# Kernel optimization log

Measured on AMD Instinct MI355X. Metric: run time of the kernel, lower is better.

The kernel has to match this reference:

```python
import jax, jax.numpy as jnp
import numpy as np

N_NODES = 50000
N_EDGES = 1250000
D_FEAT = 64


def setup_inputs() -> dict:
    key = jax.random.key(0)
    k1, k2, k3, k4 = jax.random.split(key, 4)
    feat = jax.random.normal(k1, (N_NODES, D_FEAT), dtype=jnp.float32)
    edge_weight = jax.random.uniform(k2, (N_EDGES,), dtype=jnp.float32)
    edge_src = jax.random.randint(k3, (N_EDGES,), 0, N_NODES, dtype=jnp.int64)
    edge_dst = jnp.sort(jax.random.randint(k4, (N_EDGES,), 0, N_NODES, dtype=jnp.int64))
    return {"feat": feat, "edge_weight": edge_weight,
            "edge_src": edge_src, "edge_dst": edge_dst}


def reference(feat, edge_weight, edge_src, edge_dst):
    # u_mul_e: gather source node features, scale by per-edge weight
    msgs = feat[edge_src] * edge_weight[:, None]          # [E, d]
    # fn.sum: scatter-add messages to destination nodes
    rst = jax.ops.segment_sum(msgs, edge_dst, num_segments=N_NODES)  # [N, d]
    return rst
```

## Files before the change

kernel.cpp:

```cpp
#include <hip/hip_runtime.h>

#define D_FEAT 64

__global__ __launch_bounds__(256) void build_rowptr_scatter(
    const int* __restrict__ edge_dst, int* __restrict__ rp,
    int n_edges, int n_nodes) {
  const int e = blockIdx.x * blockDim.x + threadIdx.x;
  if (e > n_edges) return;
  const int d0 = (e == 0) ? -1 : edge_dst[e - 1];
  const int d1 = (e == n_edges) ? n_nodes : edge_dst[e];
  for (int v = d0 + 1; v <= d1; ++v) rp[v] = e;
}

__global__ __launch_bounds__(256) void gcn_gather4(
    const float* __restrict__ feat,
    const float* __restrict__ ew,
    const int* __restrict__ esrc,
    const int* __restrict__ rp,
    float* __restrict__ out, int n_nodes) {
  const int wave = (blockIdx.x * blockDim.x + threadIdx.x) >> 6;
  const int lane = threadIdx.x & 63;
  if (wave >= n_nodes) return;
  const int sub = lane >> 4;
  const int fl  = lane & 15;

  const int e0 = rp[wave];
  const int e1 = rp[wave + 1];

  float4 acc0 = {0.f, 0.f, 0.f, 0.f};
  float4 acc1 = {0.f, 0.f, 0.f, 0.f};

  const float4* feat4 = (const float4*)feat;

  for (int base = e0; base < e1; base += 64) {
    const int n = min(64, e1 - base);
    int   s = 0;
    float w = 0.0f;
    if (lane < n) {
      s = esrc[base + lane];
      w = ew[base + lane];
    }
    for (int i = 0; i < n; i += 8) {
      const int   sA = __shfl(s, i + sub);
      const float wA = __shfl(w, i + sub);
      const int   sB = __shfl(s, i + 4 + sub);
      const float wB = __shfl(w, i + 4 + sub);
      const float4 rA = feat4[(size_t)sA * 16 + fl];
      const float4 rB = feat4[(size_t)sB * 16 + fl];
      acc0.x = fmaf(rA.x, wA, acc0.x);
      acc0.y = fmaf(rA.y, wA, acc0.y);
      acc0.z = fmaf(rA.z, wA, acc0.z);
      acc0.w = fmaf(rA.w, wA, acc0.w);
      acc1.x = fmaf(rB.x, wB, acc1.x);
      acc1.y = fmaf(rB.y, wB, acc1.y);
      acc1.z = fmaf(rB.z, wB, acc1.z);
      acc1.w = fmaf(rB.w, wB, acc1.w);
    }
  }

  float4 acc;
  acc.x = acc0.x + acc1.x;
  acc.y = acc0.y + acc1.y;
  acc.z = acc0.z + acc1.z;
  acc.w = acc0.w + acc1.w;

  acc.x += __shfl_xor(acc.x, 16);
  acc.y += __shfl_xor(acc.y, 16);
  acc.z += __shfl_xor(acc.z, 16);
  acc.w += __shfl_xor(acc.w, 16);
  acc.x += __shfl_xor(acc.x, 32);
  acc.y += __shfl_xor(acc.y, 32);
  acc.z += __shfl_xor(acc.z, 32);
  acc.w += __shfl_xor(acc.w, 32);

  if (lane < 16) {
    ((float4*)(out + (size_t)wave * D_FEAT))[fl] = acc;
  }
}

extern "C" void kernel_launch(void* const* d_in, const int* in_sizes, int n_in,
                              void* d_out, int out_size, void* d_ws, size_t ws_size,
                              hipStream_t stream) {
  const float* feat        = (const float*)d_in[0];
  const float* edge_weight = (const float*)d_in[1];
  const int*   edge_src    = (const int*)d_in[2];
  const int*   edge_dst    = (const int*)d_in[3];
  float* out = (float*)d_out;

  const int n_edges = in_sizes[1];
  const int n_nodes = out_size / D_FEAT;

  int* rp = (int*)d_ws;

  const int bp_threads = n_edges + 1;
  build_rowptr_scatter<<<(bp_threads + 255) / 256, 256, 0, stream>>>(
      edge_dst, rp, n_edges, n_nodes);

  const int total_threads = n_nodes * 64;
  gcn_gather4<<<(total_threads + 255) / 256, 256, 0, stream>>>(
      feat, edge_weight, edge_src, rp, out, n_nodes);
}
```

Before: 113.6 us.

## Split each node's feature columns across four waves in the gather kernel

Each destination node is now handled by four waves, one per 16-float column block, instead of one wave covering all 64 features. Within a wave, 16 edges are processed at once with 4 lanes per edge, and the inner loop is fully unrolled over a fixed 64-edge chunk. The aim is more waves in flight and more independent gathers per wave, to hide the latency of the irregular feature loads. The cost is four times as many reads of the edge index and weight arrays. Padding lanes still issue loads of row 0 with zero weight, and the reduction needs more shuffle steps.

```diff
diff --git a/kernel.cpp b/kernel.cpp
--- a/kernel.cpp
+++ b/kernel.cpp
@@ -12,24 +12,26 @@
   for (int v = d0 + 1; v <= d1; ++v) rp[v] = e;
 }
 
-__global__ __launch_bounds__(256) void gcn_gather4(
+__global__ __launch_bounds__(256) void gcn_gather_cb(
     const float* __restrict__ feat,
     const float* __restrict__ ew,
     const int* __restrict__ esrc,
     const int* __restrict__ rp,
     float* __restrict__ out, int n_nodes) {
-  const int wave = (blockIdx.x * blockDim.x + threadIdx.x) >> 6;
+  const int wid  = threadIdx.x >> 6;
   const int lane = threadIdx.x & 63;
-  if (wave >= n_nodes) return;
-  const int sub = lane >> 4;
-  const int fl  = lane & 15;
+  const int cb   = blockIdx.x & 3;
+  const int node = (blockIdx.x >> 2) * 4 + wid;
+  if (node >= n_nodes) return;
 
-  const int e0 = rp[wave];
-  const int e1 = rp[wave + 1];
+  const int slot = lane >> 2;
+  const int f4   = lane & 3;
+  const int coff = cb * 4 + f4;
 
-  float4 acc0 = {0.f, 0.f, 0.f, 0.f};
-  float4 acc1 = {0.f, 0.f, 0.f, 0.f};
+  const int e0 = rp[node];
+  const int e1 = rp[node + 1];
 
+  float4 acc = {0.f, 0.f, 0.f, 0.f};
   const float4* feat4 = (const float4*)feat;
 
   for (int base = e0; base < e1; base += 64) {
@@ -40,41 +42,29 @@
       s = esrc[base + lane];
       w = ew[base + lane];
     }
-    for (int i = 0; i < n; i += 8) {
-      const int   sA = __shfl(s, i + sub);
-      const float wA = __shfl(w, i + sub);
-      const int   sB = __shfl(s, i + 4 + sub);
-      const float wB = __shfl(w, i + 4 + sub);
-      const float4 rA = feat4[(size_t)sA * 16 + fl];
-      const float4 rB = feat4[(size_t)sB * 16 + fl];
-      acc0.x = fmaf(rA.x, wA, acc0.x);
-      acc0.y = fmaf(rA.y, wA, acc0.y);
-      acc0.z = fmaf(rA.z, wA, acc0.z);
-      acc0.w = fmaf(rA.w, wA, acc0.w);
-      acc1.x = fmaf(rB.x, wB, acc1.x);
-      acc1.y = fmaf(rB.y, wB, acc1.y);
-      acc1.z = fmaf(rB.z, wB, acc1.z);
-      acc1.w = fmaf(rB.w, wB, acc1.w);
+#pragma unroll
+    for (int i = 0; i < 64; i += 16) {
+      const int   sk = __shfl(s, i + slot);
+      const float wk = __shfl(w, i + slot);
+      const float4 q = feat4[(size_t)sk * 16 + coff];
+      acc.x = fmaf(q.x, wk, acc.x);
+      acc.y = fmaf(q.y, wk, acc.y);
+      acc.z = fmaf(q.z, wk, acc.z);
+      acc.w = fmaf(q.w, wk, acc.w);
     }
   }
 
-  float4 acc;
-  acc.x = acc0.x + acc1.x;
-  acc.y = acc0.y + acc1.y;
-  acc.z = acc0.z + acc1.z;
-  acc.w = acc0.w + acc1.w;
+  acc.x += __shfl_xor(acc.x, 4);  acc.y += __shfl_xor(acc.y, 4);
+  acc.z += __shfl_xor(acc.z, 4);  acc.w += __shfl_xor(acc.w, 4);
+  acc.x += __shfl_xor(acc.x, 8);  acc.y += __shfl_xor(acc.y, 8);
+  acc.z += __shfl_xor(acc.z, 8);  acc.w += __shfl_xor(acc.w, 8);
+  acc.x += __shfl_xor(acc.x, 16); acc.y += __shfl_xor(acc.y, 16);
+  acc.z += __shfl_xor(acc.z, 16); acc.w += __shfl_xor(acc.w, 16);
+  acc.x += __shfl_xor(acc.x, 32); acc.y += __shfl_xor(acc.y, 32);
+  acc.z += __shfl_xor(acc.z, 32); acc.w += __shfl_xor(acc.w, 32);
 
-  acc.x += __shfl_xor(acc.x, 16);
-  acc.y += __shfl_xor(acc.y, 16);
-  acc.z += __shfl_xor(acc.z, 16);
-  acc.w += __shfl_xor(acc.w, 16);
-  acc.x += __shfl_xor(acc.x, 32);
-  acc.y += __shfl_xor(acc.y, 32);
-  acc.z += __shfl_xor(acc.z, 32);
-  acc.w += __shfl_xor(acc.w, 32);
-
-  if (lane < 16) {
-    ((float4*)(out + (size_t)wave * D_FEAT))[fl] = acc;
+  if (lane < 4) {
+    ((float4*)(out + (size_t)node * D_FEAT))[coff] = acc;
   }
 }
 
@@ -96,7 +86,8 @@
   build_rowptr_scatter<<<(bp_threads + 255) / 256, 256, 0, stream>>>(
       edge_dst, rp, n_edges, n_nodes);
 
-  const int total_threads = n_nodes * 64;
-  gcn_gather4<<<(total_threads + 255) / 256, 256, 0, stream>>>(
+  const int node_groups = (n_nodes + 3) / 4;
+  const int blocks = node_groups * 4;
+  gcn_gather_cb<<<blocks, 256, 0, stream>>>(
       feat, edge_weight, edge_src, rp, out, n_nodes);
 }
```

Measured after the change: 133.6 us. 17.7% more time.
